# Kernel tuning notes

Measured on AMD Instinct MI355X. Metric: run time of the kernel, lower is better.

Reference implementation:

```python
import jax, jax.numpy as jnp
import numpy as np

N, IN, OUT = 1024, 256, 256

def setup_inputs() -> dict:
    key = jax.random.key(0)
    ks = jax.random.split(key, 8)
    hl = jax.random.normal(ks[0], (N, IN), jnp.float32)
    # hr >= hl so (hl, hr) is a valid interval input
    hr = hl + jax.random.uniform(ks[1], (N, IN), jnp.float32)
    u = lambda k, shape: jax.random.uniform(k, shape, jnp.float32, 0.02, 0.05)  # matches reset_parameters init
    w_b = u(ks[2], (IN, OUT))
    w_a = u(ks[3], (IN, OUT))
    w_c = u(ks[4], (IN, OUT))
    b_b = u(ks[5], (1, OUT))
    b_a = u(ks[6], (1, OUT))
    b_c = u(ks[7], (1, OUT))
    return {"hl": hl, "hr": hr, "w_b": w_b, "w_a": w_a, "w_c": w_c, "b_b": b_b, "b_a": b_a, "b_c": b_c}

def reference(hl, hr, w_b, w_a, w_c, b_b, b_a, b_c):
    # limit_parameters: relu on the spread parameters
    w_a = jax.nn.relu(w_a)
    w_c = jax.nn.relu(w_c)
    b_a = jax.nn.relu(b_a)
    b_c = jax.nn.relu(b_c)
    # interval weight / bias endpoints
    w_l = w_b - w_a  # [IN, OUT]
    w_r = w_b + w_c
    b_l = b_b - b_a  # [1, OUT]
    b_r = b_b + b_c
    # interval matmul: per (n,k,j) take min/max of 4 endpoint products, sum over k.
    # (Equivalent to torch interval_prod's expand/reshape/stack/min/max/sum.)
    xl = hl[:, :, None]  # [N, IN, 1]
    xr = hr[:, :, None]
    p1 = xl * w_l[None]  # [N, IN, OUT]
    p2 = xl * w_r[None]
    p3 = xr * w_l[None]
    p4 = xr * w_r[None]
    out_l = jnp.sum(jnp.minimum(jnp.minimum(p1, p2), jnp.minimum(p3, p4)), axis=1) + b_l
    out_r = jnp.sum(jnp.maximum(jnp.maximum(p1, p2), jnp.maximum(p3, p4)), axis=1) + b_r
    return (out_l, out_r)
```

## Files before the change

### kernel.cpp

```cpp
#include <hip/hip_runtime.h>

#define NN     1024
#define IN_D   256
#define OUT_D  256
#define BN     4
#define NI2    (IN_D / 2)
#define NG     8
#define JPG    (NI2 / NG)
#define OSLOTS (OUT_D / 2)

typedef float v2f __attribute__((ext_vector_type(2)));
typedef float v4f __attribute__((ext_vector_type(4)));

#define WLR_BYTES (sizeof(float4) * NI2 * OUT_D)

__global__ __launch_bounds__(256) void fz_prep(
    const float* __restrict__ wb, const float* __restrict__ wa,
    const float* __restrict__ wc, float4* __restrict__ wlr2) {
    int t = blockIdx.x * 256 + threadIdx.x;
    int ii2 = t >> 8;
    int o   = t & (OUT_D - 1);
    int i0  = (2 * ii2) * OUT_D + o;
    int i1  = i0 + OUT_D;
    float4 w;
    w.x = wb[i0] - fmaxf(wa[i0], 0.0f);
    w.y = wb[i0] + fmaxf(wc[i0], 0.0f);
    w.z = wb[i1] - fmaxf(wa[i1], 0.0f);
    w.w = wb[i1] + fmaxf(wc[i1], 0.0f);
    wlr2[t] = w;
}

template <bool PREP>
__global__ __launch_bounds__(1024) void fz_main(
    const float* __restrict__ hl, const float* __restrict__ hr,
    const float* __restrict__ wb, const float* __restrict__ wa,
    const float* __restrict__ wc, const float4* __restrict__ wlr2,
    const float* __restrict__ bb, const float* __restrict__ ba,
    const float* __restrict__ bc, float* __restrict__ out) {
    __shared__ __align__(16) v2f ab[BN][IN_D];
    __shared__ __align__(16) v2f pl[NG - 1][BN][2][OSLOTS];

    const int tid   = threadIdx.x;
    const int oslot = tid & (OSLOTS - 1);
    const int g     = tid >> 7;
    const int n0    = blockIdx.x * BN;

    {
        int row = tid >> 8;
        int ii  = tid & (IN_D - 1);
        v2f v; v.x = hl[(n0 + row) * IN_D + ii];
        v.y = hr[(n0 + row) * IN_D + ii];
        ab[row][ii] = v;
    }
    __syncthreads();

    v2f acc[BN][2];
#pragma unroll
    for (int t = 0; t < BN; ++t) {
        acc[t][0].x = 0.0f; acc[t][0].y = 0.0f;
        acc[t][1].x = 0.0f; acc[t][1].y = 0.0f;
    }

    const int j0 = g * JPG;
    const float4* wp0 = wlr2 + (size_t)j0 * OUT_D + oslot;
    const float4* wp1 = wp0 + OSLOTS;

#pragma unroll 4
    for (int j = 0; j < JPG; ++j) {
        float4 w0, w1;
        if (PREP) {
            w0 = wp0[(size_t)j * OUT_D];
            w1 = wp1[(size_t)j * OUT_D];
        } else {
            int base = (j0 + j) * 2 * OUT_D;
            int i00 = base + oslot, i01 = i00 + OUT_D;
            w0.x = wb[i00] - fmaxf(wa[i00], 0.0f);
            w0.y = wb[i00] + fmaxf(wc[i00], 0.0f);
            w0.z = wb[i01] - fmaxf(wa[i01], 0.0f);
            w0.w = wb[i01] + fmaxf(wc[i01], 0.0f);
            int i10 = base + oslot + OSLOTS, i11 = i10 + OUT_D;
            w1.x = wb[i10] - fmaxf(wa[i10], 0.0f);
            w1.y = wb[i10] + fmaxf(wc[i10], 0.0f);
            w1.z = wb[i11] - fmaxf(wa[i11], 0.0f);
            w1.w = wb[i11] + fmaxf(wc[i11], 0.0f);
        }
        const int ii = (j0 + j) * 2;
#pragma unroll
        for (int t = 0; t < BN; ++t) {
            v4f a4 = *reinterpret_cast<const v4f*>(&ab[t][ii]);
            v2f p0; p0.x = a4.x; p0.y = a4.y;
            v2f p1; p1.x = a4.z; p1.y = a4.w;
            {
                v2f l = p0 * w0.x, r = p0 * w0.y;
                v2f mm; mm.x = fminf(fminf(l.x, l.y), r.x);
                mm.y = fmaxf(fmaxf(l.x, l.y), r.y);
                acc[t][0] += mm;
            }
            {
                v2f l = p1 * w0.z, r = p1 * w0.w;
                v2f mm; mm.x = fminf(fminf(l.x, l.y), r.x);
                mm.y = fmaxf(fmaxf(l.x, l.y), r.y);
                acc[t][0] += mm;
            }
            {
                v2f l = p0 * w1.x, r = p0 * w1.y;
                v2f mm; mm.x = fminf(fminf(l.x, l.y), r.x);
                mm.y = fmaxf(fmaxf(l.x, l.y), r.y);
                acc[t][1] += mm;
            }
            {
                v2f l = p1 * w1.z, r = p1 * w1.w;
                v2f mm; mm.x = fminf(fminf(l.x, l.y), r.x);
                mm.y = fmaxf(fmaxf(l.x, l.y), r.y);
                acc[t][1] += mm;
            }
        }
    }

    if (g > 0) {
#pragma unroll
        for (int t = 0; t < BN; ++t) {
            pl[g - 1][t][0][oslot] = acc[t][0];
            pl[g - 1][t][1][oslot] = acc[t][1];
        }
    }
    __syncthreads();
    if (g == 0) {
        const int o0 = oslot, o1 = oslot + OSLOTS;
        float bl0 = bb[o0] - fmaxf(ba[o0], 0.0f);
        float br0 = bb[o0] + fmaxf(bc[o0], 0.0f);
        float bl1 = bb[o1] - fmaxf(ba[o1], 0.0f);
        float br1 = bb[o1] + fmaxf(bc[o1], 0.0f);
#pragma unroll
        for (int t = 0; t < BN; ++t) {
            v2f s0 = acc[t][0], s1 = acc[t][1];
#pragma unroll
            for (int gg = 0; gg < NG - 1; ++gg) {
                s0 += pl[gg][t][0][oslot];
                s1 += pl[gg][t][1][oslot];
            }
            size_t rl = (size_t)(n0 + t) * OUT_D;
            size_t rr = (size_t)NN * OUT_D + rl;
            out[rl + o0] = s0.x + bl0;
            out[rr + o0] = s0.y + br0;
            out[rl + o1] = s1.x + bl1;
            out[rr + o1] = s1.y + br1;
        }
    }
}

extern "C" void kernel_launch(void* const* d_in, const int* in_sizes, int n_in,
                              void* d_out, int out_size, void* d_ws, size_t ws_size,
                              hipStream_t stream) {
    const float* hl = (const float*)d_in[0];
    const float* hr = (const float*)d_in[1];
    const float* wb = (const float*)d_in[2];
    const float* wa = (const float*)d_in[3];
    const float* wc = (const float*)d_in[4];
    const float* bb = (const float*)d_in[5];
    const float* ba = (const float*)d_in[6];
    const float* bc = (const float*)d_in[7];
    float* out = (float*)d_out;

    dim3 grid(NN / BN);

    if (ws_size >= WLR_BYTES) {
        float4* wlr2 = (float4*)d_ws;
        fz_prep<<<(NI2 * OUT_D) / 256, 256, 0, stream>>>(wb, wa, wc, wlr2);
        fz_main<true><<<grid, 1024, 0, stream>>>(hl, hr, wb, wa, wc, wlr2,
                                                 bb, ba, bc, out);
    } else {
        fz_main<false><<<grid, 1024, 0, stream>>>(hl, hr, wb, wa, wc, nullptr,
                                                  bb, ba, bc, out);
    }
}
```

Before: 25.54 us.

## Fuse weight-endpoint prep into main kernel and parallelize cross-group reduction

Drops the separate prep kernel that precomputed interval weight endpoints into workspace. The main kernel now reads wb/wa/wc directly and computes the endpoints inline. This removes one launch and the workspace round trip, at the cost of three loads per weight instead of one float4 and redundant endpoint arithmetic in every block. The final reduction also changes: all 8 groups write partials to shared memory, and 4 groups each reduce one row instead of group 0 reducing all rows.

After: 27.06 us. 5.9% more time.

```diff
diff --git a/kernel.cpp b/kernel.cpp
--- a/kernel.cpp
+++ b/kernel.cpp
@@ -12,33 +12,24 @@
 typedef float v2f __attribute__((ext_vector_type(2)));
 typedef float v4f __attribute__((ext_vector_type(4)));
 
-#define WLR_BYTES (sizeof(float4) * NI2 * OUT_D)
-
-__global__ __launch_bounds__(256) void fz_prep(
-    const float* __restrict__ wb, const float* __restrict__ wa,
-    const float* __restrict__ wc, float4* __restrict__ wlr2) {
-    int t = blockIdx.x * 256 + threadIdx.x;
-    int ii2 = t >> 8;
-    int o   = t & (OUT_D - 1);
-    int i0  = (2 * ii2) * OUT_D + o;
-    int i1  = i0 + OUT_D;
-    float4 w;
-    w.x = wb[i0] - fmaxf(wa[i0], 0.0f);
-    w.y = wb[i0] + fmaxf(wc[i0], 0.0f);
-    w.z = wb[i1] - fmaxf(wa[i1], 0.0f);
-    w.w = wb[i1] + fmaxf(wc[i1], 0.0f);
-    wlr2[t] = w;
+__device__ __forceinline__ v2f wlr_of(const float* __restrict__ wb,
+                                      const float* __restrict__ wa,
+                                      const float* __restrict__ wc, int idx) {
+    float b = wb[idx];
+    v2f w;
+    w.x = b - fmaxf(wa[idx], 0.0f);
+    w.y = b + fmaxf(wc[idx], 0.0f);
+    return w;
 }
 
-template <bool PREP>
-__global__ __launch_bounds__(1024) void fz_main(
+__global__ __launch_bounds__(1024) void fz_fused(
     const float* __restrict__ hl, const float* __restrict__ hr,
     const float* __restrict__ wb, const float* __restrict__ wa,
-    const float* __restrict__ wc, const float4* __restrict__ wlr2,
+    const float* __restrict__ wc,
     const float* __restrict__ bb, const float* __restrict__ ba,
     const float* __restrict__ bc, float* __restrict__ out) {
     __shared__ __align__(16) v2f ab[BN][IN_D];
-    __shared__ __align__(16) v2f pl[NG - 1][BN][2][OSLOTS];
+    __shared__ __align__(16) v2f pl[NG][BN][2][OSLOTS];
 
     const int tid   = threadIdx.x;
     const int oslot = tid & (OSLOTS - 1);
@@ -62,90 +53,67 @@
     }
 
     const int j0 = g * JPG;
-    const float4* wp0 = wlr2 + (size_t)j0 * OUT_D + oslot;
-    const float4* wp1 = wp0 + OSLOTS;
 
 #pragma unroll 4
     for (int j = 0; j < JPG; ++j) {
-        float4 w0, w1;
-        if (PREP) {
-            w0 = wp0[(size_t)j * OUT_D];
-            w1 = wp1[(size_t)j * OUT_D];
-        } else {
-            int base = (j0 + j) * 2 * OUT_D;
-            int i00 = base + oslot, i01 = i00 + OUT_D;
-            w0.x = wb[i00] - fmaxf(wa[i00], 0.0f);
-            w0.y = wb[i00] + fmaxf(wc[i00], 0.0f);
-            w0.z = wb[i01] - fmaxf(wa[i01], 0.0f);
-            w0.w = wb[i01] + fmaxf(wc[i01], 0.0f);
-            int i10 = base + oslot + OSLOTS, i11 = i10 + OUT_D;
-            w1.x = wb[i10] - fmaxf(wa[i10], 0.0f);
-            w1.y = wb[i10] + fmaxf(wc[i10], 0.0f);
-            w1.z = wb[i11] - fmaxf(wa[i11], 0.0f);
-            w1.w = wb[i11] + fmaxf(wc[i11], 0.0f);
-        }
+        const int base = (j0 + j) * 2 * OUT_D + oslot;
+        v2f w00 = wlr_of(wb, wa, wc, base);
+        v2f w01 = wlr_of(wb, wa, wc, base + OSLOTS);
+        v2f w10 = wlr_of(wb, wa, wc, base + OUT_D);
+        v2f w11 = wlr_of(wb, wa, wc, base + OUT_D + OSLOTS);
+
         const int ii = (j0 + j) * 2;
 #pragma unroll
         for (int t = 0; t < BN; ++t) {
             v4f a4 = *reinterpret_cast<const v4f*>(&ab[t][ii]);
             v2f p0; p0.x = a4.x; p0.y = a4.y;
             v2f p1; p1.x = a4.z; p1.y = a4.w;
-            {
-                v2f l = p0 * w0.x, r = p0 * w0.y;
+            {   v2f l = p0 * w00.x, r = p0 * w00.y;
                 v2f mm; mm.x = fminf(fminf(l.x, l.y), r.x);
                 mm.y = fmaxf(fmaxf(l.x, l.y), r.y);
-                acc[t][0] += mm;
-            }
-            {
-                v2f l = p1 * w0.z, r = p1 * w0.w;
+                acc[t][0] += mm; }
+            {   v2f l = p1 * w10.x, r = p1 * w10.y;
                 v2f mm; mm.x = fminf(fminf(l.x, l.y), r.x);
                 mm.y = fmaxf(fmaxf(l.x, l.y), r.y);
-                acc[t][0] += mm;
-            }
-            {
-                v2f l = p0 * w1.x, r = p0 * w1.y;
+                acc[t][0] += mm; }
+            {   v2f l = p0 * w01.x, r = p0 * w01.y;
                 v2f mm; mm.x = fminf(fminf(l.x, l.y), r.x);
                 mm.y = fmaxf(fmaxf(l.x, l.y), r.y);
-                acc[t][1] += mm;
-            }
-            {
-                v2f l = p1 * w1.z, r = p1 * w1.w;
+                acc[t][1] += mm; }
+            {   v2f l = p1 * w11.x, r = p1 * w11.y;
                 v2f mm; mm.x = fminf(fminf(l.x, l.y), r.x);
                 mm.y = fmaxf(fmaxf(l.x, l.y), r.y);
-                acc[t][1] += mm;
-            }
+                acc[t][1] += mm; }
         }
     }
 
-    if (g > 0) {
 #pragma unroll
-        for (int t = 0; t < BN; ++t) {
-            pl[g - 1][t][0][oslot] = acc[t][0];
-            pl[g - 1][t][1][oslot] = acc[t][1];
-        }
+    for (int t = 0; t < BN; ++t) {
+        pl[g][t][0][oslot] = acc[t][0];
+        pl[g][t][1][oslot] = acc[t][1];
     }
     __syncthreads();
-    if (g == 0) {
+
+    if (g < BN) {
+        const int row = g;
         const int o0 = oslot, o1 = oslot + OSLOTS;
+        v2f s0; s0.x = 0.0f; s0.y = 0.0f;
+        v2f s1; s1.x = 0.0f; s1.y = 0.0f;
+#pragma unroll
+        for (int gg = 0; gg < NG; ++gg) {
+            s0 += pl[gg][row][0][oslot];
+            s1 += pl[gg][row][1][oslot];
+        }
         float bl0 = bb[o0] - fmaxf(ba[o0], 0.0f);
         float br0 = bb[o0] + fmaxf(bc[o0], 0.0f);
         float bl1 = bb[o1] - fmaxf(ba[o1], 0.0f);
         float br1 = bb[o1] + fmaxf(bc[o1], 0.0f);
-#pragma unroll
-        for (int t = 0; t < BN; ++t) {
-            v2f s0 = acc[t][0], s1 = acc[t][1];
-#pragma unroll
-            for (int gg = 0; gg < NG - 1; ++gg) {
-                s0 += pl[gg][t][0][oslot];
-                s1 += pl[gg][t][1][oslot];
-            }
-            size_t rl = (size_t)(n0 + t) * OUT_D;
-            size_t rr = (size_t)NN * OUT_D + rl;
-            out[rl + o0] = s0.x + bl0;
-            out[rr + o0] = s0.y + br0;
-            out[rl + o1] = s1.x + bl1;
-            out[rr + o1] = s1.y + br1;
-        }
+        size_t rl = (size_t)(n0 + row) * OUT_D;
+        size_t rr = (size_t)NN * OUT_D + rl;
+        out[rl + o0] = s0.x + bl0;
+        out[rr + o0] = s0.y + br0;
+        out[rl + o1] = s1.x + bl1;
+        out[rr + o1] = s1.y + br1;
     }
 }
 
@@ -162,15 +130,6 @@
     const float* bc = (const float*)d_in[7];
     float* out = (float*)d_out;
 
-    dim3 grid(NN / BN);
-
-    if (ws_size >= WLR_BYTES) {
-        float4* wlr2 = (float4*)d_ws;
-        fz_prep<<<(NI2 * OUT_D) / 256, 256, 0, stream>>>(wb, wa, wc, wlr2);
-        fz_main<true><<<grid, 1024, 0, stream>>>(hl, hr, wb, wa, wc, wlr2,
+    fz_fused<<<dim3(NN / BN), 1024, 0, stream>>>(hl, hr, wb, wa, wc,
                                                  bb, ba, bc, out);
-    } else {
-        fz_main<false><<<grid, 1024, 0, stream>>>(hl, hr, wb, wa, wc, nullptr,
-                                                  bb, ba, bc, out);
-    }
 }
```
